# Performance work log

Measured on AMD Instinct MI355X. Metric: run time of the kernel, lower is better.

## Reference

```python
import jax, jax.numpy as jnp
import numpy as np

VOCAB = 50257
IN_DIM = 512
NUM_CONCEPTS = 512
N_TOKENS = 131072
COMMITMENT_COST = 0.25
HINGE_MARGIN = 1.0
PDIST_EPS = 1e-6  # torch.nn.PairwiseDistance default eps (added to the diff)


def setup_inputs() -> dict:
    key = jax.random.key(0)
    k1, k2, k3, k4 = jax.random.split(key, 4)
    input_document = jax.random.randint(k1, (N_TOKENS,), 0, VOCAB)
    emb_weight = jax.random.normal(k2, (VOCAB, IN_DIM), dtype=jnp.float32) * 0.02
    # emb_concept.weight.data.uniform_(-1/K, 1/K)
    emb_concept_weight = jax.random.uniform(
        k3, (NUM_CONCEPTS, IN_DIM), dtype=jnp.float32,
        minval=-1.0 / NUM_CONCEPTS, maxval=1.0 / NUM_CONCEPTS)
    q2v_weight = jax.random.normal(k4, (VOCAB, IN_DIM), dtype=jnp.float32) * 0.02
    q2v_bias = jnp.zeros((VOCAB,), dtype=jnp.float32)
    return {"input_document": input_document, "emb_weight": emb_weight,
            "emb_concept_weight": emb_concept_weight,
            "q2v_weight": q2v_weight, "q2v_bias": q2v_bias}


def reference(input_document, emb_weight, emb_concept_weight, q2v_weight, q2v_bias):
    V, D = emb_weight.shape
    K = emb_concept_weight.shape[0]
    dtype = emb_weight.dtype

    # emb.weight.requires_grad = False in the torch module -> frozen lookup
    x = jax.lax.stop_gradient(emb_weight)[input_document]  # [N, D]

    d2 = (jnp.sum(x * x, axis=1, keepdims=True)
          + jnp.sum(emb_concept_weight * emb_concept_weight, axis=1)
          - 2.0 * (x @ emb_concept_weight.T))
    encoding_indices = jnp.argmin(d2, axis=1)              # [N]
    encodings = jax.nn.one_hot(encoding_indices, K, dtype=dtype)  # thetas [N, K]
    # encodings @ codebook == gather of codebook rows (same math, same vjp)
    quantized = jnp.take(emb_concept_weight, encoding_indices, axis=0)  # [N, D]

    e_latent = jnp.mean((jax.lax.stop_gradient(quantized) - x) ** 2)
    q_latent = jnp.mean((quantized - jax.lax.stop_gradient(x)) ** 2)
    vq_loss = q_latent + COMMITMENT_COST * e_latent

    quantized_words = x + jax.lax.stop_gradient(quantized - x)  # straight-through
    quantized_docu = jnp.mean(quantized_words, axis=0, keepdims=True)  # [1, D]

    # calc_loss_lts(): hinge loss on all KxK pairwise distances
    # dist[i,j] = || c_i - c_j + eps ||_2, expanded without gathering K^2 pairs:
    s = jnp.sum(emb_concept_weight, axis=1)                 # [K]
    n = jnp.sum(emb_concept_weight * emb_concept_weight, axis=1)  # [K]
    G = emb_concept_weight @ emb_concept_weight.T           # [K, K]
    dd = (n[:, None] + n[None, :] - 2.0 * G
          + 2.0 * PDIST_EPS * (s[:, None] - s[None, :])
          + D * (PDIST_EPS * PDIST_EPS))
    dist = jnp.sqrt(jnp.maximum(dd, 0.0))
    diag = jnp.eye(K, dtype=bool)
    # HingeEmbeddingLoss: label +1 (i==j) -> d ; label -1 -> max(0, margin - d)
    lts_loss = jnp.mean(jnp.where(diag, dist, jnp.maximum(0.0, HINGE_MARGIN - dist)))

    logits = quantized_docu @ q2v_weight.T + q2v_bias       # [1, V]
    outputs = jnp.log(jax.nn.softmax(logits, axis=1) + 1e-6)
    bin_count = jnp.zeros((V,), dtype=dtype).at[input_document].add(1.0)
    outputs = outputs * bin_count                           # [1, V]

    return encodings, quantized_words, quantized_docu, outputs, vq_loss, lts_loss
```

## Files before the change

### kernel.cpp

```cpp
#include <hip/hip_runtime.h>
#include <math.h>

#define N_TOK 131072
#define VOCAB 50257
#define DIM   512
#define K_CON 512
#define NPARTS 12565

#define OFF_ENC  ((size_t)0)
#define OFF_QW   ((size_t)67108864)
#define OFF_DOCU ((size_t)134217728)
#define OFF_OUT  ((size_t)134218240)
#define OFF_VQ   ((size_t)134268497)
#define OFF_LTS  ((size_t)134268498)

#define WS_COUNTS 0
#define WS_VQ     2048
#define WS_LTS    2056
#define WS_SUMV   2072
#define WS_NFLAG  2080
#define WS_NARR   4096
#define WS_SARR   6144
#define WS_BINC   8192
#define WS_LOGITS 209920
#define WS_FLAGS  411648
#define WS_PART   544768
#define FLAG_CAP  32768

typedef __attribute__((ext_vector_type(4)))  float f32x4;
typedef __attribute__((ext_vector_type(8)))  _Float16 f16x8;
typedef __attribute__((ext_vector_type(16))) float f32x16;

__device__ _Float16 g_B1[32 * 2 * 512 * 8];
__device__ _Float16 g_A16[(size_t)VOCAB * DIM];
__device__ float g_NW[VOCAB];

__device__ inline void gload16(const void* g, void* l) {
    __builtin_amdgcn_global_load_lds(
        (const __attribute__((address_space(1))) unsigned int*)g,
        (__attribute__((address_space(3))) unsigned int*)l, 16, 0, 0);
}

__global__ void k_nsprep(const float* __restrict__ cw, float* __restrict__ n_arr,
                         float* __restrict__ s_arr, _Float16* __restrict__ b1,
                         uint4* __restrict__ wz) {
    if (blockIdx.x == 0) {
        uint4 z; z.x = 0u; z.y = 0u; z.z = 0u; z.w = 0u;
        wz[threadIdx.x] = z;
    }
    int w = threadIdx.x >> 6, lane = threadIdx.x & 63;
    int r = blockIdx.x * 4 + w;
    const float* row = cw + (size_t)r * DIM;
    {
        float4 a = *(const float4*)(row + lane * 8);
        float4 b = *(const float4*)(row + lane * 8 + 4);
        float v[8] = {a.x,a.y,a.z,a.w,b.x,b.y,b.z,b.w};
        double na = 0.0, sa = 0.0;
        #pragma unroll
        for (int e = 0; e < 8; ++e) { na += (double)v[e]*v[e]; sa += (double)v[e]; }
        for (int off = 32; off; off >>= 1) {
            na += __shfl_down(na, off);
            sa += __shfl_down(sa, off);
        }
        if (lane == 0) { n_arr[r] = (float)na; s_arr[r] = (float)sa; }
    }
    {
        int s = lane >> 1, hf = lane & 1;
        const float* p = row + s * 16 + hf * 8;
        float4 xa = *(const float4*)p;
        float4 xb = *(const float4*)(p + 4);
        float xf[8] = {xa.x,xa.y,xa.z,xa.w,xb.x,xb.y,xb.z,xb.w};
        f16x8 h8;
        #pragma unroll
        for (int e = 0; e < 8; ++e) h8[e] = (_Float16)(xf[e] * 512.0f);
        *(f16x8*)&b1[(((size_t)s * 2 + hf) * 512 + r) * 8] = h8;
    }
}

__global__ void k_prepa(const float* __restrict__ emb, _Float16* __restrict__ a16,
                        float* __restrict__ nw, unsigned* __restrict__ binc) {
    int wv = threadIdx.x >> 6, lane = threadIdx.x & 63;
    int r = blockIdx.x * 4 + wv;
    if (r >= VOCAB) return;
    const float* row = emb + (size_t)r * DIM;
    float4 a = *(const float4*)(row + lane * 8);
    float4 b = *(const float4*)(row + lane * 8 + 4);
    float v[8] = {a.x,a.y,a.z,a.w,b.x,b.y,b.z,b.w};
    f16x8 h;
    double na = 0.0;
    #pragma unroll
    for (int e = 0; e < 8; ++e) { h[e] = (_Float16)v[e]; na += (double)v[e]*v[e]; }
    *(f16x8*)&a16[(size_t)r * DIM + lane * 8] = h;
    for (int off = 32; off; off >>= 1) na += __shfl_down(na, off);
    if (lane == 0) { nw[r] = (float)na; binc[r] = 0u; }
}

__global__ __launch_bounds__(512, 4)
void k_main(const int* __restrict__ doc, const float* __restrict__ cw,
            const float* __restrict__ n_arr,
            float* __restrict__ out, unsigned* __restrict__ counts,
            unsigned* __restrict__ binc,
            double* __restrict__ vq_acc, unsigned* __restrict__ nflag,
            unsigned* __restrict__ flag_list) {
    __shared__ f16x8 bsh[4][1024];
    __shared__ float nsl[512];
    __shared__ float nxs[64];
    __shared__ uint4 redv[8][64];
    __shared__ int docs[64];
    __shared__ int idxs[64];
    __shared__ double dred[512];

    const int tid   = threadIdx.x;
    const int n0    = blockIdx.x * 64;
    const int lane  = tid & 63;
    const int wv    = tid >> 6;
    const int wm    = wv >> 2;
    const int wq    = wv & 3;
    const int hv    = lane >> 5;
    const int ln31  = lane & 31;
    const int cbase = wq * 128 + ln31;

    if (tid < 64) docs[tid] = doc[n0 + tid];
    nsl[tid] = n_arr[tid];
    __syncthreads();

#define STAGE16(P, DST)                                                       \
    {                                                                         \
        const char* srcb = (const char*)g_B1 + (size_t)(P) * 16384;           \
        char* dstb = (char*)(DST);                                            \
        gload16(srcb + tid * 16, dstb + tid * 16);                            \
        gload16(srcb + 8192 + tid * 16, dstb + 8192 + tid * 16);              \
    }

    const char* aptr = (const char*)(g_A16 + (size_t)docs[wm * 32 + ln31] * DIM);

    STAGE16(0, bsh[0]);
    STAGE16(1, bsh[1]);
    STAGE16(2, bsh[2]);
    f16x8 x0 = *(const f16x8*)(aptr + (hv * 8) * 2);
    f16x8 x1 = *(const f16x8*)(aptr + (16 + hv * 8) * 2);
    f16x8 x2 = *(const f16x8*)(aptr + (32 + hv * 8) * 2);
    if (tid < 64) nxs[tid] = g_NW[docs[tid]];
    __syncthreads();

    f32x16 acc[4];
    #pragma unroll
    for (int n = 0; n < 4; ++n) acc[n] = (f32x16)(0.0f);

    #pragma unroll
    for (int p = 0; p < 32; ++p) {
        if (p >= 1) {
            __builtin_amdgcn_sched_barrier(0);
            if (p <= 29)      asm volatile("s_waitcnt vmcnt(6)" ::: "memory");
            else if (p == 30) asm volatile("s_waitcnt vmcnt(3)" ::: "memory");
            else              asm volatile("s_waitcnt vmcnt(0)" ::: "memory");
            __builtin_amdgcn_sched_barrier(0);
            __builtin_amdgcn_s_barrier();
            __builtin_amdgcn_sched_barrier(0);
        }
        f16x8 na = x2;
        if (p + 3 < 32) {
            na = *(const f16x8*)(aptr + ((p + 3) * 16 + hv * 8) * 2);
            __builtin_amdgcn_sched_barrier(0);
            STAGE16(p + 3, bsh[(p + 3) & 3]);
            __builtin_amdgcn_sched_barrier(0);
        }
        const f16x8* bb = bsh[p & 3];
        #pragma unroll
        for (int n = 0; n < 4; ++n) {
            f16x8 b = bb[hv * 512 + cbase + n * 32];
            acc[n] = __builtin_amdgcn_mfma_f32_32x32x16_f16(x0, b, acc[n], 0, 0, 0);
        }
        x0 = x1; x1 = x2; x2 = na;
    }
#undef STAGE16
    __syncthreads();

    float nsv[4];
    #pragma unroll
    for (int n = 0; n < 4; ++n) nsv[n] = nsl[cbase + n * 32];

    #pragma unroll
    for (int r = 0; r < 16; ++r) {
        int tt = (r & 3) + ((r >> 2) << 3) + (hv << 2);
        float nxr = nxs[wm * 32 + tt];
        float v1 = INFINITY, v2 = INFINITY; int j1 = 0x7fffffff;
        #pragma unroll
        for (int n = 0; n < 4; ++n) {
            float d = fmaf(-0.00390625f, acc[n][r], nxr + nsv[n]);
            int jj = cbase + n * 32;
            if (d < v1) { v2 = v1; v1 = d; j1 = jj; }
            else if (d < v2) { v2 = d; }
        }
        #pragma unroll
        for (int off = 1; off < 32; off <<= 1) {
            float ov1 = __shfl_xor(v1, off);
            int   oj1 = __shfl_xor(j1, off);
            float ov2 = __shfl_xor(v2, off);
            v2 = fminf(fminf(v2, ov2), fmaxf(v1, ov1));
            bool take = (ov1 < v1) || (ov1 == v1 && oj1 < j1);
            if (take) { v1 = ov1; j1 = oj1; }
        }
        if (ln31 == 0)
            redv[wv][wm * 32 + tt] = make_uint4(__float_as_uint(v1), (unsigned)j1,
                                                __float_as_uint(v2), 0u);
    }
    __syncthreads();
    double myv1 = 0.0;
    if (tid < 64) {
        int g = tid >> 5;
        uint4 a = redv[g * 4][tid];
        float v1 = __uint_as_float(a.x), v2 = __uint_as_float(a.z);
        int j1 = (int)a.y;
        #pragma unroll
        for (int w = 1; w < 4; ++w) {
            uint4 b = redv[g * 4 + w][tid];
            float wv1 = __uint_as_float(b.x), wv2 = __uint_as_float(b.z);
            v2 = fminf(fminf(v2, wv2), fmaxf(v1, wv1));
            bool take = (wv1 < v1) || (wv1 == v1 && (int)b.y < j1);
            if (take) { v1 = wv1; j1 = (int)b.y; }
        }
        idxs[tid] = j1;
        atomicAdd(&counts[j1], 1u);
        atomicAdd(&binc[docs[tid]], 1u);
        myv1 = (double)v1;
        if (v2 - v1 <= 2e-6f) {
            unsigned pq = atomicAdd(nflag, 1u);
            if (pq < FLAG_CAP) flag_list[pq] = (unsigned)(n0 + tid);
        }
    }
    dred[tid] = myv1;
    __syncthreads();

    for (int lin = tid; lin < 8192; lin += 512) {
        int t = lin >> 7, f4 = lin & 127;
        int idx = idxs[t];
        int b4 = f4 << 2;
        f32x4 v;
        v.x = (idx == b4)     ? 1.f : 0.f;
        v.y = (idx == b4 + 1) ? 1.f : 0.f;
        v.z = (idx == b4 + 2) ? 1.f : 0.f;
        v.w = (idx == b4 + 3) ? 1.f : 0.f;
        __builtin_nontemporal_store(v,
            (f32x4*)(out + OFF_ENC + ((size_t)(n0 + t) << 9) + (size_t)b4));
    }
    for (int lin = tid; lin < 8192; lin += 512) {
        int t = lin >> 7, f4 = lin & 127;
        f32x4 c4 = *(const f32x4*)(cw + (size_t)idxs[t] * DIM + (f4 << 2));
        __builtin_nontemporal_store(c4,
            (f32x4*)(out + OFF_QW + ((size_t)(n0 + t) << 9) + (size_t)(f4 << 2)));
    }
    for (int st = 256; st; st >>= 1) {
        if (tid < st) dred[tid] += dred[tid + st];
        __syncthreads();
    }
    if (tid == 0) atomicAdd(vq_acc, dred[0]);
}

__global__ __launch_bounds__(512)
void k_fixup(const int* __restrict__ doc, const float* __restrict__ emb,
             const float* __restrict__ cw, const float* __restrict__ n_arr,
             const float* __restrict__ nw,
             const unsigned* __restrict__ nflag, const unsigned* __restrict__ flag_list,
             float* __restrict__ out, unsigned* __restrict__ counts,
             double* __restrict__ vq_acc) {
    __shared__ float4 xs4[128];
    __shared__ int oldj_sh;
    __shared__ float vsh[512];
    __shared__ unsigned long long keys[512];

    const int tid = threadIdx.x;
    unsigned nf = *nflag;
    if (nf > FLAG_CAP) nf = FLAG_CAP;

    for (unsigned f = blockIdx.x; f < nf; f += gridDim.x) {
        int t = (int)flag_list[f];
        int dc = doc[t];
        float nxf = nw[dc];
        if (tid < 128)
            xs4[tid] = *(const float4*)(emb + (size_t)dc * DIM + tid * 4);
        if (tid == 0) oldj_sh = -1;
        __syncthreads();
        {
            float e = out[OFF_ENC + (size_t)t * 512 + tid];
            if (e == 1.0f) oldj_sh = tid;
        }
        {
            const float4* cr = (const float4*)(cw + (size_t)tid * DIM);
            float acc = 0.f;
            #pragma unroll 8
            for (int fq = 0; fq < 128; ++fq) {
                float4 c4 = cr[fq], x4 = xs4[fq];
                acc = fmaf(x4.x, c4.x, acc);
                acc = fmaf(x4.y, c4.y, acc);
                acc = fmaf(x4.z, c4.z, acc);
                acc = fmaf(x4.w, c4.w, acc);
            }
            float v = fmaf(-2.f, acc, nxf + n_arr[tid]);
            vsh[tid] = v;
            keys[tid] = (((unsigned long long)__float_as_uint(v)) << 32) | (unsigned)tid;
        }
        __syncthreads();
        for (int st = 256; st; st >>= 1) {
            if (tid < st) {
                unsigned long long o = keys[tid + st];
                if (o < keys[tid]) keys[tid] = o;
            }
            __syncthreads();
        }
        int newj = (int)(keys[0] & 0xffffffffu);
        int oldj = oldj_sh;
        if (newj != oldj) {
            if (tid == 0) {
                out[OFF_ENC + (size_t)t * 512 + oldj] = 0.0f;
                out[OFF_ENC + (size_t)t * 512 + newj] = 1.0f;
                atomicSub(&counts[oldj], 1u);
                atomicAdd(&counts[newj], 1u);
                atomicAdd(vq_acc, (double)vsh[newj] - (double)vsh[oldj]);
            }
            if (tid < 128) {
                float4 cn = *(const float4*)(cw + (size_t)newj * DIM + tid * 4);
                *(float4*)&out[OFF_QW + (size_t)t * 512 + tid * 4] = cn;
            }
        }
        __syncthreads();
    }
}

__global__ void k_docu(const unsigned* __restrict__ counts,
                       const float* __restrict__ cw, float* __restrict__ out_docu) {
    __shared__ float cnt[512];
    int tid = threadIdx.x;
    cnt[tid] = (float)counts[tid];
    __syncthreads();
    double a = 0.0;
    for (int j = 0; j < K_CON; ++j)
        a += (double)cnt[j] * (double)cw[(size_t)j * DIM + tid];
    out_docu[tid] = (float)(a * (1.0 / (double)N_TOK));
}

__global__ __launch_bounds__(256)
void k_ltsm(const float* __restrict__ n_arr, const float* __restrict__ s_arr,
            double* __restrict__ lts_acc) {
    const int tid  = threadIdx.x;
    const int lane = tid & 63;
    const int wv   = tid >> 6;
    const int hv   = lane >> 5;
    const int ln31 = lane & 31;
    const int tile = blockIdx.x * 4 + wv;
    const int ti = tile >> 4, tj = tile & 15;

    const f16x8* bt = (const f16x8*)g_B1;
    f32x16 acc = (f32x16)(0.0f);
    #pragma unroll
    for (int s = 0; s < 32; ++s) {
        f16x8 af = bt[((size_t)s * 2 + hv) * 512 + ti * 32 + ln31];
        f16x8 bf = bt[((size_t)s * 2 + hv) * 512 + tj * 32 + ln31];
        acc = __builtin_amdgcn_mfma_f32_32x32x16_f16(af, bf, acc, 0, 0, 0);
    }

    const int j = tj * 32 + ln31;
    const float nj = n_arr[j], sj = s_arr[j];
    const float EPS = 1e-6f;
    double lsum = 0.0;
    #pragma unroll
    for (int r = 0; r < 16; ++r) {
        int row = (r & 3) + ((r >> 2) << 3) + (hv << 2);
        int i = ti * 32 + row;
        float ddv = n_arr[i] + nj
                  + fmaf(-2.0f / 262144.0f, acc[r],
                         2.f * EPS * (s_arr[i] - sj) + 512.f * EPS * EPS);
        float dist = sqrtf(fmaxf(ddv, 0.f));
        lsum += (double)((i == j) ? dist : fmaxf(0.f, 1.f - dist));
    }
    for (int off = 32; off; off >>= 1) lsum += __shfl_down(lsum, off);
    if (lane == 0) atomicAdd(lts_acc, lsum);
}

__global__ void k_logexp(const float* __restrict__ docu, const float* __restrict__ q2w,
                         const float* __restrict__ q2b, float* __restrict__ evals,
                         double* __restrict__ parts) {
    __shared__ double esh[4];
    int wvi = threadIdx.x >> 6, lane = threadIdx.x & 63;
    int v = blockIdx.x * 4 + wvi;
    if (lane == 0) esh[wvi] = 0.0;
    if (v < VOCAB) {
        const float* wr = q2w + (size_t)v * DIM;
        float4 a = *(const float4*)(wr + lane*8);
        float4 b = *(const float4*)(wr + lane*8 + 4);
        float4 da = *(const float4*)(docu + lane*8);
        float4 db = *(const float4*)(docu + lane*8 + 4);
        float p = a.x*da.x + a.y*da.y + a.z*da.z + a.w*da.w
                + b.x*db.x + b.y*db.y + b.z*db.z + b.w*db.w;
        for (int off = 32; off; off >>= 1) p += __shfl_down(p, off);
        if (lane == 0) {
            float e = expf(p + q2b[v]);
            evals[v] = e;
            esh[wvi] = (double)e;
        }
    }
    __syncthreads();
    if (threadIdx.x == 0)
        parts[blockIdx.x] = esh[0] + esh[1] + esh[2] + esh[3];
}

__global__ void k_sumred(const double* __restrict__ parts, double* __restrict__ sumv) {
    __shared__ double red[256];
    int tid = threadIdx.x;
    double s = 0.0;
    for (int i = tid; i < NPARTS; i += 256) s += parts[i];
    red[tid] = s; __syncthreads();
    for (int st = 128; st; st >>= 1) {
        if (tid < st) red[tid] += red[tid + st];
        __syncthreads();
    }
    if (tid == 0) *sumv = red[0];
}

__global__ void k_final(const float* __restrict__ evals,
                        const double* __restrict__ sumv, const unsigned* __restrict__ binc,
                        const double* __restrict__ vq_acc, const double* __restrict__ lts_acc,
                        float* __restrict__ out) {
    int v = blockIdx.x * 256 + threadIdx.x;
    if (v < VOCAB) {
        float s = (float)(*sumv);
        float p = evals[v] / s;
        out[OFF_OUT + v] = logf(p + 1e-6f) * (float)binc[v];
    }
    if (v == 0) {
        out[OFF_VQ]  = (float)(1.25 * (*vq_acc) * (1.0 / 67108864.0));
        out[OFF_LTS] = (float)((*lts_acc) * (1.0 / 262144.0));
    }
}

extern "C" void kernel_launch(void* const* d_in, const int* in_sizes, int n_in,
                              void* d_out, int out_size, void* d_ws, size_t ws_size,
                              hipStream_t stream) {
    const int*   doc = (const int*)d_in[0];
    const float* emb = (const float*)d_in[1];
    const float* cw  = (const float*)d_in[2];
    const float* q2w = (const float*)d_in[3];
    const float* q2b = (const float*)d_in[4];
    float* out = (float*)d_out;
    char* ws = (char*)d_ws;

    unsigned* counts = (unsigned*)(ws + WS_COUNTS);
    double*   vq_acc = (double*)(ws + WS_VQ);
    double*   lts_acc= (double*)(ws + WS_LTS);
    double*   sumv   = (double*)(ws + WS_SUMV);
    unsigned* nflag  = (unsigned*)(ws + WS_NFLAG);
    float*    n_arr  = (float*)(ws + WS_NARR);
    float*    s_arr  = (float*)(ws + WS_SARR);
    unsigned* binc   = (unsigned*)(ws + WS_BINC);
    float*    evals  = (float*)(ws + WS_LOGITS);
    unsigned* flags  = (unsigned*)(ws + WS_FLAGS);
    double*   parts  = (double*)(ws + WS_PART);

    _Float16* b1;  hipGetSymbolAddress((void**)&b1,  HIP_SYMBOL(g_B1));
    _Float16* a16; hipGetSymbolAddress((void**)&a16, HIP_SYMBOL(g_A16));
    float*    nw;  hipGetSymbolAddress((void**)&nw,  HIP_SYMBOL(g_NW));


    hipLaunchKernelGGL(k_nsprep, dim3(128),   dim3(256), 0, stream, cw, n_arr, s_arr,
                       b1, (uint4*)ws);
    hipLaunchKernelGGL(k_prepa,  dim3(NPARTS), dim3(256), 0, stream, emb, a16, nw, binc);
    hipLaunchKernelGGL(k_main,   dim3(2048),  dim3(512), 0, stream, doc, cw, n_arr,
                       out, counts, binc, vq_acc, nflag, flags);
    hipLaunchKernelGGL(k_fixup,  dim3(2048),  dim3(512), 0, stream, doc, emb, cw, n_arr,
                       nw, nflag, flags, out, counts, vq_acc);
    hipLaunchKernelGGL(k_docu,   dim3(1),     dim3(512), 0, stream, counts, cw, out + OFF_DOCU);
    hipLaunchKernelGGL(k_ltsm,   dim3(64),    dim3(256), 0, stream, n_arr, s_arr, lts_acc);
    hipLaunchKernelGGL(k_logexp, dim3(NPARTS), dim3(256), 0, stream,
                       out + OFF_DOCU, q2w, q2b, evals, parts);
    hipLaunchKernelGGL(k_sumred, dim3(1), dim3(256), 0, stream, parts, sumv);
    hipLaunchKernelGGL(k_final,  dim3((VOCAB + 255) / 256), dim3(256), 0, stream,
                       evals, sumv, binc, vq_acc, lts_acc, out);
}
```

Measured before the change: 380.8 us.

## Double token tile per block in k_main to reuse staged codebook tiles

Each k_main block now handles 128 tokens instead of 64. Every wave computes two 32-row MFMA accumulator sets that share the same LDS-staged codebook fragment, so global-to-LDS codebook traffic per token is halved, and the grid is halved to match. The cost is twice as many accumulator registers, which is why launch bounds drop to 2 blocks per CU. That may reduce occupancy and latency hiding, and with 1024 blocks the grid may cover the CUs less evenly.

```diff
diff --git a/kernel.cpp b/kernel.cpp
--- a/kernel.cpp
+++ b/kernel.cpp
@@ -95,7 +95,7 @@
     if (lane == 0) { nw[r] = (float)na; binc[r] = 0u; }
 }
 
-__global__ __launch_bounds__(512, 4)
+__global__ __launch_bounds__(512, 2)
 void k_main(const int* __restrict__ doc, const float* __restrict__ cw,
             const float* __restrict__ n_arr,
             float* __restrict__ out, unsigned* __restrict__ counts,
@@ -104,14 +104,14 @@
             unsigned* __restrict__ flag_list) {
     __shared__ f16x8 bsh[4][1024];
     __shared__ float nsl[512];
-    __shared__ float nxs[64];
+    __shared__ float nxs[128];
     __shared__ uint4 redv[8][64];
-    __shared__ int docs[64];
-    __shared__ int idxs[64];
+    __shared__ int docs[128];
+    __shared__ int idxs[128];
     __shared__ double dred[512];
 
     const int tid   = threadIdx.x;
-    const int n0    = blockIdx.x * 64;
+    const int n0    = blockIdx.x * 128;
     const int lane  = tid & 63;
     const int wv    = tid >> 6;
     const int wm    = wv >> 2;
@@ -120,7 +120,7 @@
     const int ln31  = lane & 31;
     const int cbase = wq * 128 + ln31;
 
-    if (tid < 64) docs[tid] = doc[n0 + tid];
+    if (tid < 128) docs[tid] = doc[n0 + tid];
     nsl[tid] = n_arr[tid];
     __syncthreads();
 
@@ -132,35 +132,40 @@
         gload16(srcb + 8192 + tid * 16, dstb + 8192 + tid * 16);              \
     }
 
-    const char* aptr = (const char*)(g_A16 + (size_t)docs[wm * 32 + ln31] * DIM);
+    const char* aptrA = (const char*)(g_A16 + (size_t)docs[wm * 64 + ln31] * DIM);
+    const char* aptrB = (const char*)(g_A16 + (size_t)docs[wm * 64 + 32 + ln31] * DIM);
 
     STAGE16(0, bsh[0]);
     STAGE16(1, bsh[1]);
     STAGE16(2, bsh[2]);
-    f16x8 x0 = *(const f16x8*)(aptr + (hv * 8) * 2);
-    f16x8 x1 = *(const f16x8*)(aptr + (16 + hv * 8) * 2);
-    f16x8 x2 = *(const f16x8*)(aptr + (32 + hv * 8) * 2);
-    if (tid < 64) nxs[tid] = g_NW[docs[tid]];
-    __syncthreads();
-
-    f32x16 acc[4];
-    #pragma unroll
-    for (int n = 0; n < 4; ++n) acc[n] = (f32x16)(0.0f);
+    f16x8 x0a = *(const f16x8*)(aptrA + (hv * 8) * 2);
+    f16x8 x1a = *(const f16x8*)(aptrA + (16 + hv * 8) * 2);
+    f16x8 x2a = *(const f16x8*)(aptrA + (32 + hv * 8) * 2);
+    f16x8 x0b = *(const f16x8*)(aptrB + (hv * 8) * 2);
+    f16x8 x1b = *(const f16x8*)(aptrB + (16 + hv * 8) * 2);
+    f16x8 x2b = *(const f16x8*)(aptrB + (32 + hv * 8) * 2);
+    if (tid < 128) nxs[tid] = g_NW[docs[tid]];
+    __syncthreads();
+
+    f32x16 accA[4], accB[4];
+    #pragma unroll
+    for (int n = 0; n < 4; ++n) { accA[n] = (f32x16)(0.0f); accB[n] = (f32x16)(0.0f); }
 
     #pragma unroll
     for (int p = 0; p < 32; ++p) {
         if (p >= 1) {
             __builtin_amdgcn_sched_barrier(0);
-            if (p <= 29)      asm volatile("s_waitcnt vmcnt(6)" ::: "memory");
-            else if (p == 30) asm volatile("s_waitcnt vmcnt(3)" ::: "memory");
+            if (p <= 29)      asm volatile("s_waitcnt vmcnt(8)" ::: "memory");
+            else if (p == 30) asm volatile("s_waitcnt vmcnt(4)" ::: "memory");
             else              asm volatile("s_waitcnt vmcnt(0)" ::: "memory");
             __builtin_amdgcn_sched_barrier(0);
             __builtin_amdgcn_s_barrier();
             __builtin_amdgcn_sched_barrier(0);
         }
-        f16x8 na = x2;
+        f16x8 naA = x2a, naB = x2b;
         if (p + 3 < 32) {
-            na = *(const f16x8*)(aptr + ((p + 3) * 16 + hv * 8) * 2);
+            naA = *(const f16x8*)(aptrA + ((p + 3) * 16 + hv * 8) * 2);
+            naB = *(const f16x8*)(aptrB + ((p + 3) * 16 + hv * 8) * 2);
             __builtin_amdgcn_sched_barrier(0);
             STAGE16(p + 3, bsh[(p + 3) & 3]);
             __builtin_amdgcn_sched_barrier(0);
@@ -169,9 +174,11 @@
         #pragma unroll
         for (int n = 0; n < 4; ++n) {
             f16x8 b = bb[hv * 512 + cbase + n * 32];
-            acc[n] = __builtin_amdgcn_mfma_f32_32x32x16_f16(x0, b, acc[n], 0, 0, 0);
-        }
-        x0 = x1; x1 = x2; x2 = na;
+            accA[n] = __builtin_amdgcn_mfma_f32_32x32x16_f16(x0a, b, accA[n], 0, 0, 0);
+            accB[n] = __builtin_amdgcn_mfma_f32_32x32x16_f16(x0b, b, accB[n], 0, 0, 0);
+        }
+        x0a = x1a; x1a = x2a; x2a = naA;
+        x0b = x1b; x1b = x2b; x2b = naB;
     }
 #undef STAGE16
     __syncthreads();
@@ -181,40 +188,44 @@
     for (int n = 0; n < 4; ++n) nsv[n] = nsl[cbase + n * 32];
 
     #pragma unroll
-    for (int r = 0; r < 16; ++r) {
-        int tt = (r & 3) + ((r >> 2) << 3) + (hv << 2);
-        float nxr = nxs[wm * 32 + tt];
-        float v1 = INFINITY, v2 = INFINITY; int j1 = 0x7fffffff;
+    for (int g = 0; g < 2; ++g) {
+        const f32x16* am = g ? accB : accA;
         #pragma unroll
-        for (int n = 0; n < 4; ++n) {
-            float d = fmaf(-0.00390625f, acc[n][r], nxr + nsv[n]);
-            int jj = cbase + n * 32;
-            if (d < v1) { v2 = v1; v1 = d; j1 = jj; }
-            else if (d < v2) { v2 = d; }
-        }
-        #pragma unroll
-        for (int off = 1; off < 32; off <<= 1) {
-            float ov1 = __shfl_xor(v1, off);
-            int   oj1 = __shfl_xor(j1, off);
-            float ov2 = __shfl_xor(v2, off);
-            v2 = fminf(fminf(v2, ov2), fmaxf(v1, ov1));
-            bool take = (ov1 < v1) || (ov1 == v1 && oj1 < j1);
-            if (take) { v1 = ov1; j1 = oj1; }
-        }
-        if (ln31 == 0)
-            redv[wv][wm * 32 + tt] = make_uint4(__float_as_uint(v1), (unsigned)j1,
-                                                __float_as_uint(v2), 0u);
+        for (int r = 0; r < 16; ++r) {
+            int tt = (r & 3) + ((r >> 2) << 3) + (hv << 2);
+            float nxr = nxs[wm * 64 + g * 32 + tt];
+            float v1 = INFINITY, v2 = INFINITY; int j1 = 0x7fffffff;
+            #pragma unroll
+            for (int n = 0; n < 4; ++n) {
+                float d = fmaf(-0.00390625f, am[n][r], nxr + nsv[n]);
+                int jj = cbase + n * 32;
+                if (d < v1) { v2 = v1; v1 = d; j1 = jj; }
+                else if (d < v2) { v2 = d; }
+            }
+            #pragma unroll
+            for (int off = 1; off < 32; off <<= 1) {
+                float ov1 = __shfl_xor(v1, off);
+                int   oj1 = __shfl_xor(j1, off);
+                float ov2 = __shfl_xor(v2, off);
+                v2 = fminf(fminf(v2, ov2), fmaxf(v1, ov1));
+                bool take = (ov1 < v1) || (ov1 == v1 && oj1 < j1);
+                if (take) { v1 = ov1; j1 = oj1; }
+            }
+            if (ln31 == 0)
+                redv[wv][g * 32 + tt] = make_uint4(__float_as_uint(v1), (unsigned)j1,
+                                                   __float_as_uint(v2), 0u);
+        }
     }
     __syncthreads();
     double myv1 = 0.0;
-    if (tid < 64) {
-        int g = tid >> 5;
-        uint4 a = redv[g * 4][tid];
+    if (tid < 128) {
+        int wmt = tid >> 6, loc = tid & 63;
+        uint4 a = redv[wmt * 4][loc];
         float v1 = __uint_as_float(a.x), v2 = __uint_as_float(a.z);
         int j1 = (int)a.y;
         #pragma unroll
         for (int w = 1; w < 4; ++w) {
-            uint4 b = redv[g * 4 + w][tid];
+            uint4 b = redv[wmt * 4 + w][loc];
             float wv1 = __uint_as_float(b.x), wv2 = __uint_as_float(b.z);
             v2 = fminf(fminf(v2, wv2), fmaxf(v1, wv1));
             bool take = (wv1 < v1) || (wv1 == v1 && (int)b.y < j1);
@@ -232,7 +243,7 @@
     dred[tid] = myv1;
     __syncthreads();
 
-    for (int lin = tid; lin < 8192; lin += 512) {
+    for (int lin = tid; lin < 16384; lin += 512) {
         int t = lin >> 7, f4 = lin & 127;
         int idx = idxs[t];
         int b4 = f4 << 2;
@@ -244,7 +255,7 @@
         __builtin_nontemporal_store(v,
             (f32x4*)(out + OFF_ENC + ((size_t)(n0 + t) << 9) + (size_t)b4));
     }
-    for (int lin = tid; lin < 8192; lin += 512) {
+    for (int lin = tid; lin < 16384; lin += 512) {
         int t = lin >> 7, f4 = lin & 127;
         f32x4 c4 = *(const f32x4*)(cw + (size_t)idxs[t] * DIM + (f4 << 2));
         __builtin_nontemporal_store(c4,
@@ -464,7 +475,7 @@
     hipLaunchKernelGGL(k_nsprep, dim3(128),   dim3(256), 0, stream, cw, n_arr, s_arr,
                        b1, (uint4*)ws);
     hipLaunchKernelGGL(k_prepa,  dim3(NPARTS), dim3(256), 0, stream, emb, a16, nw, binc);
-    hipLaunchKernelGGL(k_main,   dim3(2048),  dim3(512), 0, stream, doc, cw, n_arr,
+    hipLaunchKernelGGL(k_main,   dim3(1024),  dim3(512), 0, stream, doc, cw, n_arr,
                        out, counts, binc, vq_acc, nflag, flags);
     hipLaunchKernelGGL(k_fixup,  dim3(2048),  dim3(512), 0, stream, doc, emb, cw, n_arr,
                        nw, nflag, flags, out, counts, vq_acc);
```

After: 449.3 us. 1.18x slower.
